# Kernel optimization log

Measured on AMD Instinct MI355X. Metric: run time of the kernel, lower is better.

The kernel has to match this reference:

```python
import math
import jax
import jax.numpy as jnp
import numpy as np


def _db2_synthesis_kernel():
    """Build the fused separable synthesis kernel, HWIO (4,4,4,1).

    Faithful to the source: the first conv acts along width (fw), the second
    (after transpose) along height (fh). NOTE: the original code applies
    db2_lpf (not hpf) as the second filter for the LH band -- we replicate
    that exactly.
    """
    s = math.sqrt(3.0)
    d = 4.0 * math.sqrt(2.0)
    h0 = (1.0 + s) / d
    h1 = (3.0 + s) / d
    h2 = (3.0 - s) / d
    h3 = (1.0 - s) / d
    lpf = jnp.array([h3, h2, h1, h0], dtype=jnp.float32)
    hpf = jnp.array([-h0, h1, -h2, h3], dtype=jnp.float32)
    # (height_filter, width_filter) per input channel [LL, LH, HL, HH]
    pairs = [(lpf, lpf), (lpf, lpf), (lpf, hpf), (hpf, hpf)]
    # K[p, q, c, 0] = fh_c[p] * fw_c[q]; summing over c fuses the 4 subband adds
    K = jnp.stack([jnp.outer(fh, fw) for fh, fw in pairs], axis=2)[..., None]
    return K  # (4, 4, 4, 1)


def setup_inputs() -> dict:
    key = jax.random.key(0)
    x = jax.random.normal(key, (32, 512, 512, 4), dtype=jnp.float32)
    return {"x": x}


def reference(x):
    # x: [B, H, W, 4] wavelet subbands (LL, LH, HL, HH)
    K = _db2_synthesis_kernel()
    # symmetric pad of 3 on each spatial side, as in the source
    xp = jnp.pad(x, ((0, 0), (3, 3), (3, 3), (0, 0)), mode="symmetric")
    # zero-upsample-by-2 + 4-tap separable filter bank, expressed as a single
    # lhs-dilated conv. lhs_dilation=2 inserts zeros BETWEEN samples (length
    # 2n-1); the TF upsampler appends one trailing zero row/col (length 2n),
    # so pad (0,1) on each spatial dim before the VALID window.
    y = jax.lax.conv_general_dilated(
        xp, K,
        window_strides=(1, 1),
        padding=((0, 1), (0, 1)),
        lhs_dilation=(2, 2),
        dimension_numbers=("NHWC", "HWIO", "NHWC"),
    )  # [B, 2(H+6)-3, 2(W+6)-3, 1]
    return y[:, 5:-4, 5:-4, :]  # [B, 2H, 2W, 1]
```

## Files before the change

### kernel.cpp

```cpp
#include <hip/hip_runtime.h>

constexpr float h0 = 0.48296291314469025f;
constexpr float h1 = 0.83651630373746900f;
constexpr float h2 = 0.22414386804185735f;
constexpr float h3 = -0.12940952255092145f;


__global__ __launch_bounds__(256) void idwt_kernel(const float4* __restrict__ x,
                                                   float4* __restrict__ out) {
    const int idx = blockIdx.x * blockDim.x + threadIdx.x;
    const int np = idx & 255;
    const int t = idx >> 8;
    const int m = t & 511;
    const int b = t >> 9;

    const int n0 = np << 1;
    const int n2 = (n0 + 2 < 512) ? n0 + 2 : 511;
    const int mB = (m < 511) ? m + 1 : 511;

    const size_t rowA = (size_t)((b << 9) + m) * 512;
    const size_t rowB = (size_t)((b << 9) + mB) * 512;

    const float4 pA0 = x[rowA + n0], pA1 = x[rowA + n0 + 1], pA2 = x[rowA + n2];
    const float4 pB0 = x[rowB + n0], pB1 = x[rowB + n0 + 1], pB2 = x[rowB + n2];

    float Lv0[3], Lv1[3], Hv0[3], Hv1[3];
    {
        const float4 pa[3] = {pA0, pA1, pA2};
        const float4 pb[3] = {pB0, pB1, pB2};
#pragma unroll
        for (int j = 0; j < 3; ++j) {
            const float LA = pa[j].x + pa[j].y;
            const float LB = pb[j].x + pb[j].y;
            Lv0[j] = h2 * LA + h0 * LB;
            Lv1[j] = h3 * LA + h1 * LB;
            Hv0[j] = (h2 * pa[j].z + h0 * pb[j].z) + (h1 * pa[j].w + h3 * pb[j].w);
            Hv1[j] = (h3 * pa[j].z + h1 * pb[j].z) + (-h0 * pa[j].w - h2 * pb[j].w);
        }
    }

    float4 r0, r1;
    r0.x = h2 * Lv0[0] + h0 * Lv0[1] + h1 * Hv0[0] + h3 * Hv0[1];
    r0.y = h3 * Lv0[0] + h1 * Lv0[1] - h0 * Hv0[0] - h2 * Hv0[1];
    r0.z = h2 * Lv0[1] + h0 * Lv0[2] + h1 * Hv0[1] + h3 * Hv0[2];
    r0.w = h3 * Lv0[1] + h1 * Lv0[2] - h0 * Hv0[1] - h2 * Hv0[2];
    r1.x = h2 * Lv1[0] + h0 * Lv1[1] + h1 * Hv1[0] + h3 * Hv1[1];
    r1.y = h3 * Lv1[0] + h1 * Lv1[1] - h0 * Hv1[0] - h2 * Hv1[1];
    r1.z = h2 * Lv1[1] + h0 * Lv1[2] + h1 * Hv1[1] + h3 * Hv1[2];
    r1.w = h3 * Lv1[1] + h1 * Lv1[2] - h0 * Hv1[1] - h2 * Hv1[2];

    const size_t o0 = (size_t)((b << 10) + (m << 1)) * 256 + np;
    out[o0]       = r0;
    out[o0 + 256] = r1;
}

extern "C" void kernel_launch(void* const* d_in, const int* in_sizes, int n_in,
                              void* d_out, int out_size, void* d_ws, size_t ws_size,
                              hipStream_t stream) {
    const float4* x = (const float4*)d_in[0];
    float4* out = (float4*)d_out;
    const int total = 32 * 512 * 256;
    idwt_kernel<<<total / 256, 256, 0, stream>>>(x, out);
}
```

Measured before the change: 222.0 us.

## Process four output row-pairs per thread and swizzle block order across XCDs

Each thread now produces four consecutive row-pairs, loading five input rows instead of two rows per row-pair, so overlapping input rows are reused in registers instead of being fetched again. Block indices are remapped so each group of eight interleaved blocks maps to contiguous chunks, presumably to keep neighbouring rows on the same XCD's L2. This cuts redundant global reads and cache traffic, at the cost of more registers per thread and four times fewer blocks.

```diff
diff --git a/kernel.cpp b/kernel.cpp
--- a/kernel.cpp
+++ b/kernel.cpp
@@ -6,52 +6,73 @@
 constexpr float h3 = -0.12940952255092145f;
 
 
+constexpr int R = 4;
+
 __global__ __launch_bounds__(256) void idwt_kernel(const float4* __restrict__ x,
                                                    float4* __restrict__ out) {
-    const int idx = blockIdx.x * blockDim.x + threadIdx.x;
-    const int np = idx & 255;
-    const int t = idx >> 8;
-    const int m = t & 511;
-    const int b = t >> 9;
+    const int bid   = blockIdx.x;
+    const int chunk = gridDim.x >> 3;
+    const int lid   = (bid & 7) * chunk + (bid >> 3);
+
+    const int np = threadIdx.x;
+    const int t  = lid & 127;
+    const int b  = lid >> 7;
 
     const int n0 = np << 1;
     const int n2 = (n0 + 2 < 512) ? n0 + 2 : 511;
-    const int mB = (m < 511) ? m + 1 : 511;
+    const int m0 = t << 2;
 
-    const size_t rowA = (size_t)((b << 9) + m) * 512;
-    const size_t rowB = (size_t)((b << 9) + mB) * 512;
+    const size_t base = (size_t)b * (512 * 512);
 
-    const float4 pA0 = x[rowA + n0], pA1 = x[rowA + n0 + 1], pA2 = x[rowA + n2];
-    const float4 pB0 = x[rowB + n0], pB1 = x[rowB + n0 + 1], pB2 = x[rowB + n2];
+    float4 p[R + 1][3];
+#pragma unroll
+    for (int r = 0; r <= R; ++r) {
+        int mm = m0 + r;
+        mm = (mm < 512) ? mm : 511;
+        const size_t row = base + (size_t)mm * 512;
+        p[r][0] = x[row + n0];
+        p[r][1] = x[row + n0 + 1];
+        p[r][2] = x[row + n2];
+    }
 
-    float Lv0[3], Lv1[3], Hv0[3], Hv1[3];
-    {
-        const float4 pa[3] = {pA0, pA1, pA2};
-        const float4 pb[3] = {pB0, pB1, pB2};
+    float A[R + 1][3], z[R + 1][3], w[R + 1][3];
+#pragma unroll
+    for (int r = 0; r <= R; ++r) {
 #pragma unroll
         for (int j = 0; j < 3; ++j) {
-            const float LA = pa[j].x + pa[j].y;
-            const float LB = pb[j].x + pb[j].y;
-            Lv0[j] = h2 * LA + h0 * LB;
-            Lv1[j] = h3 * LA + h1 * LB;
-            Hv0[j] = (h2 * pa[j].z + h0 * pb[j].z) + (h1 * pa[j].w + h3 * pb[j].w);
-            Hv1[j] = (h3 * pa[j].z + h1 * pb[j].z) + (-h0 * pa[j].w - h2 * pb[j].w);
+            A[r][j] = p[r][j].x + p[r][j].y;
+            z[r][j] = p[r][j].z;
+            w[r][j] = p[r][j].w;
         }
     }
 
-    float4 r0, r1;
-    r0.x = h2 * Lv0[0] + h0 * Lv0[1] + h1 * Hv0[0] + h3 * Hv0[1];
-    r0.y = h3 * Lv0[0] + h1 * Lv0[1] - h0 * Hv0[0] - h2 * Hv0[1];
-    r0.z = h2 * Lv0[1] + h0 * Lv0[2] + h1 * Hv0[1] + h3 * Hv0[2];
-    r0.w = h3 * Lv0[1] + h1 * Lv0[2] - h0 * Hv0[1] - h2 * Hv0[2];
-    r1.x = h2 * Lv1[0] + h0 * Lv1[1] + h1 * Hv1[0] + h3 * Hv1[1];
-    r1.y = h3 * Lv1[0] + h1 * Lv1[1] - h0 * Hv1[0] - h2 * Hv1[1];
-    r1.z = h2 * Lv1[1] + h0 * Lv1[2] + h1 * Hv1[1] + h3 * Hv1[2];
-    r1.w = h3 * Lv1[1] + h1 * Lv1[2] - h0 * Hv1[1] - h2 * Hv1[2];
+    size_t o = (size_t)((b << 10) + (m0 << 1)) * 256 + np;
 
-    const size_t o0 = (size_t)((b << 10) + (m << 1)) * 256 + np;
-    out[o0]       = r0;
-    out[o0 + 256] = r1;
+#pragma unroll
+    for (int r = 0; r < R; ++r) {
+        float Lv0[3], Lv1[3], Hv0[3], Hv1[3];
+#pragma unroll
+        for (int j = 0; j < 3; ++j) {
+            Lv0[j] = h2 * A[r][j] + h0 * A[r + 1][j];
+            Lv1[j] = h3 * A[r][j] + h1 * A[r + 1][j];
+            Hv0[j] = (h2 * z[r][j] + h0 * z[r + 1][j]) + (h1 * w[r][j] + h3 * w[r + 1][j]);
+            Hv1[j] = (h3 * z[r][j] + h1 * z[r + 1][j]) + (-h0 * w[r][j] - h2 * w[r + 1][j]);
+        }
+
+        float4 r0, r1;
+        r0.x = h2 * Lv0[0] + h0 * Lv0[1] + h1 * Hv0[0] + h3 * Hv0[1];
+        r0.y = h3 * Lv0[0] + h1 * Lv0[1] - h0 * Hv0[0] - h2 * Hv0[1];
+        r0.z = h2 * Lv0[1] + h0 * Lv0[2] + h1 * Hv0[1] + h3 * Hv0[2];
+        r0.w = h3 * Lv0[1] + h1 * Lv0[2] - h0 * Hv0[1] - h2 * Hv0[2];
+        r1.x = h2 * Lv1[0] + h0 * Lv1[1] + h1 * Hv1[0] + h3 * Hv1[1];
+        r1.y = h3 * Lv1[0] + h1 * Lv1[1] - h0 * Hv1[0] - h2 * Hv1[1];
+        r1.z = h2 * Lv1[1] + h0 * Lv1[2] + h1 * Hv1[1] + h3 * Hv1[2];
+        r1.w = h3 * Lv1[1] + h1 * Lv1[2] - h0 * Hv1[1] - h2 * Hv1[2];
+
+        out[o]       = r0;
+        out[o + 256] = r1;
+        o += 512;
+    }
 }
 
 extern "C" void kernel_launch(void* const* d_in, const int* in_sizes, int n_in,
@@ -59,6 +80,6 @@
                               hipStream_t stream) {
     const float4* x = (const float4*)d_in[0];
     float4* out = (float4*)d_out;
-    const int total = 32 * 512 * 256;
-    idwt_kernel<<<total / 256, 256, 0, stream>>>(x, out);
+    const int blocks = 32 * 128;
+    idwt_kernel<<<blocks, 256, 0, stream>>>(x, out);
 }
```

Measured after the change: 245.9 us. 10.8% more time.

## Process eight input rows per thread to reuse loaded rows across outputs

Applied to the files above, without the earlier changes.

Each thread now walks eight consecutive input rows and keeps a sliding window of row data in registers. Neighbouring output rows share that data, so each input row is read about once instead of twice, and the grid shrinks by a factor of eight. In exchange, per-thread register use goes up and fewer threads are in flight, which may lower the latency hiding available to this memory-bound kernel.

```diff
diff --git a/kernel.cpp b/kernel.cpp
--- a/kernel.cpp
+++ b/kernel.cpp
@@ -8,50 +8,68 @@
 
 __global__ __launch_bounds__(256) void idwt_kernel(const float4* __restrict__ x,
                                                    float4* __restrict__ out) {
-    const int idx = blockIdx.x * blockDim.x + threadIdx.x;
+    const int idx = blockIdx.x * 256 + threadIdx.x;
     const int np = idx & 255;
-    const int t = idx >> 8;
-    const int m = t & 511;
-    const int b = t >> 9;
+    const int t  = idx >> 8;
+    const int s  = t & 63;
+    const int b  = t >> 6;
 
     const int n0 = np << 1;
     const int n2 = (n0 + 2 < 512) ? n0 + 2 : 511;
-    const int mB = (m < 511) ? m + 1 : 511;
+    const int m0 = s << 3;
 
-    const size_t rowA = (size_t)((b << 9) + m) * 512;
-    const size_t rowB = (size_t)((b << 9) + mB) * 512;
+    const size_t base = (size_t)(b << 9) * 512;
 
-    const float4 pA0 = x[rowA + n0], pA1 = x[rowA + n0 + 1], pA2 = x[rowA + n2];
-    const float4 pB0 = x[rowB + n0], pB1 = x[rowB + n0 + 1], pB2 = x[rowB + n2];
+    float4 row[9][3];
 
-    float Lv0[3], Lv1[3], Hv0[3], Hv1[3];
-    {
-        const float4 pa[3] = {pA0, pA1, pA2};
-        const float4 pb[3] = {pB0, pB1, pB2};
+#pragma unroll
+    for (int r = 0; r < 3; ++r) {
+        const size_t ro = base + (size_t)(m0 + r) * 512;
+        row[r][0] = x[ro + n0];
+        row[r][1] = x[ro + n0 + 1];
+        row[r][2] = x[ro + n2];
+    }
+
+    size_t o = ((size_t)(b << 10) + (size_t)(m0 << 1)) * 256 + np;
+
+#pragma unroll
+    for (int i = 0; i < 8; ++i) {
+        if (i < 6) {
+            const int mr = m0 + i + 3;
+            const int mm = (mr < 512) ? mr : 511;
+            const size_t ro = base + (size_t)mm * 512;
+            row[i + 3][0] = x[ro + n0];
+            row[i + 3][1] = x[ro + n0 + 1];
+            row[i + 3][2] = x[ro + n2];
+        }
+
+        float Lv0[3], Lv1[3], Hv0[3], Hv1[3];
 #pragma unroll
         for (int j = 0; j < 3; ++j) {
-            const float LA = pa[j].x + pa[j].y;
-            const float LB = pb[j].x + pb[j].y;
+            const float LA = row[i][j].x + row[i][j].y;
+            const float LB = row[i + 1][j].x + row[i + 1][j].y;
             Lv0[j] = h2 * LA + h0 * LB;
             Lv1[j] = h3 * LA + h1 * LB;
-            Hv0[j] = (h2 * pa[j].z + h0 * pb[j].z) + (h1 * pa[j].w + h3 * pb[j].w);
-            Hv1[j] = (h3 * pa[j].z + h1 * pb[j].z) + (-h0 * pa[j].w - h2 * pb[j].w);
+            Hv0[j] = (h2 * row[i][j].z + h0 * row[i + 1][j].z)
+                   + (h1 * row[i][j].w + h3 * row[i + 1][j].w);
+            Hv1[j] = (h3 * row[i][j].z + h1 * row[i + 1][j].z)
+                   + (-h0 * row[i][j].w - h2 * row[i + 1][j].w);
         }
+
+        float4 r0, r1;
+        r0.x = h2 * Lv0[0] + h0 * Lv0[1] + h1 * Hv0[0] + h3 * Hv0[1];
+        r0.y = h3 * Lv0[0] + h1 * Lv0[1] - h0 * Hv0[0] - h2 * Hv0[1];
+        r0.z = h2 * Lv0[1] + h0 * Lv0[2] + h1 * Hv0[1] + h3 * Hv0[2];
+        r0.w = h3 * Lv0[1] + h1 * Lv0[2] - h0 * Hv0[1] - h2 * Hv0[2];
+        r1.x = h2 * Lv1[0] + h0 * Lv1[1] + h1 * Hv1[0] + h3 * Hv1[1];
+        r1.y = h3 * Lv1[0] + h1 * Lv1[1] - h0 * Hv1[0] - h2 * Hv1[1];
+        r1.z = h2 * Lv1[1] + h0 * Lv1[2] + h1 * Hv1[1] + h3 * Hv1[2];
+        r1.w = h3 * Lv1[1] + h1 * Lv1[2] - h0 * Hv1[1] - h2 * Hv1[2];
+
+        out[o]       = r0;
+        out[o + 256] = r1;
+        o += 512;
     }
-
-    float4 r0, r1;
-    r0.x = h2 * Lv0[0] + h0 * Lv0[1] + h1 * Hv0[0] + h3 * Hv0[1];
-    r0.y = h3 * Lv0[0] + h1 * Lv0[1] - h0 * Hv0[0] - h2 * Hv0[1];
-    r0.z = h2 * Lv0[1] + h0 * Lv0[2] + h1 * Hv0[1] + h3 * Hv0[2];
-    r0.w = h3 * Lv0[1] + h1 * Lv0[2] - h0 * Hv0[1] - h2 * Hv0[2];
-    r1.x = h2 * Lv1[0] + h0 * Lv1[1] + h1 * Hv1[0] + h3 * Hv1[1];
-    r1.y = h3 * Lv1[0] + h1 * Lv1[1] - h0 * Hv1[0] - h2 * Hv1[1];
-    r1.z = h2 * Lv1[1] + h0 * Lv1[2] + h1 * Hv1[1] + h3 * Hv1[2];
-    r1.w = h3 * Lv1[1] + h1 * Lv1[2] - h0 * Hv1[1] - h2 * Hv1[2];
-
-    const size_t o0 = (size_t)((b << 10) + (m << 1)) * 256 + np;
-    out[o0]       = r0;
-    out[o0 + 256] = r1;
 }
 
 extern "C" void kernel_launch(void* const* d_in, const int* in_sizes, int n_in,
@@ -59,6 +77,6 @@
                               hipStream_t stream) {
     const float4* x = (const float4*)d_in[0];
     float4* out = (float4*)d_out;
-    const int total = 32 * 512 * 256;
-    idwt_kernel<<<total / 256, 256, 0, stream>>>(x, out);
+    const int blocks = 32 * 64 * 256 / 256;
+    idwt_kernel<<<blocks, 256, 0, stream>>>(x, out);
 }
```

After: 231.3 us. +4.2%, slower.
